# Optimization experiments

Measured on AMD Instinct MI355X. Metric: run time of the kernel, lower is better.

Reference implementation:

```python
import jax, jax.numpy as jnp
import numpy as np

B, T, V, E, H, O = 4096, 5, 8192, 32, 512, 1024
LN_EPS = 1e-5


def _ln(x, g, b):
    m = x.mean(-1, keepdims=True)
    v = x.var(-1, keepdims=True)
    return (x - m) / jnp.sqrt(v + LN_EPS) * g + b


def setup_inputs() -> dict:
    key = jax.random.key(0)
    ks = jax.random.split(key, 8)
    s_emb = 1.0 / np.sqrt(V)
    s_gru = 1.0 / np.sqrt(H)
    s_fc = 1.0 / np.sqrt(H)
    return {
        "message": jax.random.normal(ks[0], (B, T, V), jnp.float32),
        "emb_W": jax.random.normal(ks[1], (E, V), jnp.float32) * s_emb,
        "emb_b": jnp.zeros((E,), jnp.float32),
        "init_emb": jax.random.normal(ks[2], (1, E), jnp.float32),
        "eln_g": jnp.ones((E,), jnp.float32),
        "eln_b": jnp.zeros((E,), jnp.float32),
        "Wih": jax.random.normal(ks[3], (3 * H, E), jnp.float32) * s_gru,
        "Whh": jax.random.normal(ks[4], (3 * H, H), jnp.float32) * s_gru,
        "bih": jnp.zeros((3 * H,), jnp.float32),
        "bhh": jnp.zeros((3 * H,), jnp.float32),
        "gln_g": jnp.ones((H,), jnp.float32),
        "gln_b": jnp.zeros((H,), jnp.float32),
        "fc_W": jax.random.normal(ks[5], (O, H), jnp.float32) * s_fc,
        "fc_b": jnp.zeros((O,), jnp.float32),
    }


def reference(message, emb_W, emb_b, init_emb, eln_g, eln_b,
              Wih, Whh, bih, bhh, gln_g, gln_b, fc_W, fc_b):
    # embed all message steps at once: [B, T, E]
    emb = _ln(jnp.einsum('btv,ev->bte', message, emb_W) + emb_b, eln_g, eln_b)
    # GRU input sequence: LN(initial_embedding), then embeddings of steps 0..T-2
    x0 = jnp.broadcast_to(_ln(init_emb, eln_g, eln_b), (B, E))
    xs = jnp.concatenate([x0[None], jnp.swapaxes(emb[:, :T - 1], 0, 1)], axis=0)  # [T, B, E]

    def step(h, x):
        gi = x @ Wih.T + bih            # [B, 3H]
        gh = h @ Whh.T + bhh            # [B, 3H]
        ir, iz, inn = jnp.split(gi, 3, axis=-1)
        hr, hz, hn = jnp.split(gh, 3, axis=-1)
        r = jax.nn.sigmoid(ir + hr)
        z = jax.nn.sigmoid(iz + hz)
        n = jnp.tanh(inn + r * hn)
        h_new = (1.0 - z) * n + z * h
        return h_new, None

    h_last, _ = jax.lax.scan(step, jnp.zeros((B, H), message.dtype), xs)
    # eval mode: GaussianDropout is identity
    return jax.nn.sigmoid(_ln(h_last, gln_g, gln_b) @ fc_W.T + fc_b)
```

## Files before the change

kernel.cpp:

```cpp
#include <hip/hip_runtime.h>
#include <hip/hip_bf16.h>
#include <math.h>


#define LN_EPS 1e-5f

typedef __attribute__((ext_vector_type(8))) short bf8;
typedef __attribute__((ext_vector_type(4))) float fx4;

__device__ __forceinline__ float bf2f(short s) {
    union { unsigned u; float f; } v;
    v.u = ((unsigned)(unsigned short)s) << 16;
    return v.f;
}
__device__ __forceinline__ short f2bf(float f) {
    union { __hip_bfloat16 h; unsigned short u; } v;
    v.h = __float2bfloat16(f);
    return (short)v.u;
}
__device__ __forceinline__ float sigmoidf(float x) { return 1.0f / (1.0f + expf(-x)); }

__global__ __launch_bounds__(256) void k_prep(
    const float* __restrict__ Whh, const float* __restrict__ Wih,
    const float* __restrict__ fcW, const float* __restrict__ embW,
    const float* __restrict__ init_emb, const float* __restrict__ eln_g,
    const float* __restrict__ eln_b,
    short* __restrict__ Whh_bf, short* __restrict__ Wih_bf,
    short* __restrict__ fcW_bf, short* __restrict__ embW_bf,
    short* __restrict__ x0v, short* __restrict__ h0)
{
    int gid = blockIdx.x * blockDim.x + threadIdx.x;
    int stride = gridDim.x * blockDim.x;
    for (int i = gid; i < 1536 * 512; i += stride) Whh_bf[i] = f2bf(Whh[i]);
    for (int i = gid; i < 1536 * 32;  i += stride) Wih_bf[i] = f2bf(Wih[i]);
    for (int i = gid; i < 1024 * 512; i += stride) fcW_bf[i] = f2bf(fcW[i]);
    for (int i = gid; i < 32 * 8192;  i += stride) embW_bf[i] = f2bf(embW[i]);
    int* h0i = (int*)h0;
    for (int i = gid; i < 4096 * 512 / 2; i += stride) h0i[i] = 0;
    if (blockIdx.x == 0 && threadIdx.x < 32) {
        float v = init_emb[threadIdx.x];
        float s = v, q = v * v;
        #pragma unroll
        for (int m = 1; m < 32; m <<= 1) { s += __shfl_xor(s, m); q += __shfl_xor(q, m); }
        float mean = s * (1.0f / 32.0f);
        float var  = q * (1.0f / 32.0f) - mean * mean;
        float rstd = rsqrtf(var + LN_EPS);
        x0v[threadIdx.x] = f2bf((v - mean) * rstd * eln_g[threadIdx.x] + eln_b[threadIdx.x]);
    }
}

__global__ __launch_bounds__(256) void k_embed(
    const float* __restrict__ msg, const short* __restrict__ embW_bf,
    const float* __restrict__ emb_b, const float* __restrict__ eln_g,
    const float* __restrict__ eln_b, short* __restrict__ xs)
{
    __shared__ float part[4][16][33];

    const int tid  = threadIdx.x;
    const int w    = tid >> 6;
    const int lane = tid & 63;
    const int m    = lane & 15;
    const int quad = lane >> 4;

    const int rg = blockIdx.x * 16 + m;
    const int b  = rg >> 2, t = rg & 3;
    const float* __restrict__ row = msg + (size_t)(b * 5 + t) * 8192;

    const short* __restrict__ bw0 = embW_bf + (size_t)m * 8192;
    const short* __restrict__ bw1 = embW_bf + (size_t)(16 + m) * 8192;

    fx4 acc0, acc1;
    #pragma unroll
    for (int j = 0; j < 4; ++j) { acc0[j] = 0.0f; acc1[j] = 0.0f; }

    const int kbeg = w * 2048;
    const int kend = kbeg + 2048;
    #pragma unroll 4
    for (int k0 = kbeg; k0 < kend; k0 += 32) {
        const int kq = k0 + quad * 8;
        float4 a0 = *(const float4*)(row + kq);
        float4 a1 = *(const float4*)(row + kq + 4);
        bf8 a;
        a[0] = f2bf(a0.x); a[1] = f2bf(a0.y); a[2] = f2bf(a0.z); a[3] = f2bf(a0.w);
        a[4] = f2bf(a1.x); a[5] = f2bf(a1.y); a[6] = f2bf(a1.z); a[7] = f2bf(a1.w);
        bf8 b0 = *(const bf8*)(bw0 + kq);
        bf8 b1 = *(const bf8*)(bw1 + kq);
        acc0 = __builtin_amdgcn_mfma_f32_16x16x32_bf16(a, b0, acc0, 0, 0, 0);
        acc1 = __builtin_amdgcn_mfma_f32_16x16x32_bf16(a, b1, acc1, 0, 0, 0);
    }

    #pragma unroll
    for (int r = 0; r < 4; ++r) {
        part[w][quad * 4 + r][m]      = acc0[r];
        part[w][quad * 4 + r][16 + m] = acc1[r];
    }
    __syncthreads();

    {
        const int rr = tid >> 5;
        const int c  = tid & 31;
        #pragma unroll
        for (int half = 0; half < 2; ++half) {
            const int r = rr + half * 8;
            float v = part[0][r][c] + part[1][r][c] + part[2][r][c] + part[3][r][c]
                    + emb_b[c];
            float s = v, q = v * v;
            #pragma unroll
            for (int msk = 1; msk < 32; msk <<= 1) {
                s += __shfl_xor(s, msk); q += __shfl_xor(q, msk);
            }
            float mean = s * (1.0f / 32.0f);
            float var  = q * (1.0f / 32.0f) - mean * mean;
            float rstd = rsqrtf(var + LN_EPS);
            const int rg2 = blockIdx.x * 16 + r;
            const int b2 = rg2 >> 2, t2 = rg2 & 3;
            xs[(size_t)(t2 + 1) * 131072 + (size_t)b2 * 32 + c] =
                f2bf((v - mean) * rstd * eln_g[c] + eln_b[c]);
        }
    }
}

__global__ __launch_bounds__(256) void k_gru_step(
    const short* __restrict__ x, int x_stride,
    const short* __restrict__ h_in, short* __restrict__ h_out,
    const short* __restrict__ Whh_bf, const short* __restrict__ Wih_bf,
    const float* __restrict__ bih, const float* __restrict__ bhh)
{
    __shared__ short Hs[64][72];
    __shared__ short Ws[96][72];
    __shared__ short Xs[64][40];
    __shared__ short WIs[96][40];

    const int tid  = threadIdx.x;
    const int wid  = tid >> 6;
    const int lane = tid & 63;
    const int m    = lane & 15;
    const int quad = lane >> 4;
    const int row0 = blockIdx.x * 64;
    const int j0   = blockIdx.y * 32;

    fx4 acc_h[6], acc_i[6];
    #pragma unroll
    for (int i = 0; i < 6; ++i)
        #pragma unroll
        for (int j = 0; j < 4; ++j) { acc_h[i][j] = 0.0f; acc_i[i][j] = 0.0f; }

    {
        int c = tid;
        int r = c >> 2, kp = (c & 3) * 8;
        const short* src = x + (size_t)(row0 + r) * x_stride + kp;
        *(bf8*)&Xs[r][kp] = *(const bf8*)src;
    }
    #pragma unroll
    for (int i = 0; i < 2; ++i) {
        int c = tid + i * 256;
        if (c < 384) {
            int n = c >> 2, kp = (c & 3) * 8;
            int s = n >> 5, jj = n & 31;
            int g = s * 512 + j0 + jj;
            *(bf8*)&WIs[n][kp] = *(const bf8*)(Wih_bf + (size_t)g * 32 + kp);
        }
    }

    for (int k0 = 0; k0 < 512; k0 += 64) {
        #pragma unroll
        for (int i = 0; i < 2; ++i) {
            int c = tid + i * 256;
            int r = c >> 3, kp = (c & 7) * 8;
            *(bf8*)&Hs[r][kp] = *(const bf8*)(h_in + (size_t)(row0 + r) * 512 + k0 + kp);
        }
        #pragma unroll
        for (int i = 0; i < 3; ++i) {
            int c = tid + i * 256;
            int n = c >> 3, kp = (c & 7) * 8;
            int s = n >> 5, jj = n & 31;
            int g = s * 512 + j0 + jj;
            *(bf8*)&Ws[n][kp] = *(const bf8*)(Whh_bf + (size_t)g * 512 + k0 + kp);
        }
        __syncthreads();
        #pragma unroll
        for (int kk = 0; kk < 64; kk += 32) {
            bf8 a = *(const bf8*)&Hs[wid * 16 + m][kk + quad * 8];
            #pragma unroll
            for (int nt = 0; nt < 6; ++nt) {
                bf8 b = *(const bf8*)&Ws[(nt >> 1) * 32 + (nt & 1) * 16 + m][kk + quad * 8];
                acc_h[nt] = __builtin_amdgcn_mfma_f32_16x16x32_bf16(a, b, acc_h[nt], 0, 0, 0);
            }
        }
        __syncthreads();
    }
    {
        bf8 a = *(const bf8*)&Xs[wid * 16 + m][quad * 8];
        #pragma unroll
        for (int nt = 0; nt < 6; ++nt) {
            bf8 b = *(const bf8*)&WIs[(nt >> 1) * 32 + (nt & 1) * 16 + m][quad * 8];
            acc_i[nt] = __builtin_amdgcn_mfma_f32_16x16x32_bf16(a, b, acc_i[nt], 0, 0, 0);
        }
    }
    #pragma unroll
    for (int nt = 0; nt < 2; ++nt) {
        #pragma unroll
        for (int r = 0; r < 4; ++r) {
            int j  = j0 + nt * 16 + m;
            int rg = row0 + wid * 16 + quad * 4 + r;
            float rpre = acc_i[0 + nt][r] + bih[j]        + acc_h[0 + nt][r] + bhh[j];
            float zpre = acc_i[2 + nt][r] + bih[512 + j]  + acc_h[2 + nt][r] + bhh[512 + j];
            float inn  = acc_i[4 + nt][r] + bih[1024 + j];
            float hn   = acc_h[4 + nt][r] + bhh[1024 + j];
            float rr = sigmoidf(rpre);
            float zz = sigmoidf(zpre);
            float nn = tanhf(inn + rr * hn);
            float ho = bf2f(h_in[(size_t)rg * 512 + j]);
            h_out[(size_t)rg * 512 + j] = f2bf((1.0f - zz) * nn + zz * ho);
        }
    }
}

__global__ __launch_bounds__(256) void k_hln(
    const short* __restrict__ h, const float* __restrict__ g,
    const float* __restrict__ b, short* __restrict__ hln)
{
    int wid = threadIdx.x >> 6, lane = threadIdx.x & 63;
    int row = blockIdx.x * 4 + wid;
    bf8 v = *(const bf8*)(h + (size_t)row * 512 + lane * 8);
    float f[8];
    float sum = 0.f, sq = 0.f;
    #pragma unroll
    for (int i = 0; i < 8; ++i) { f[i] = bf2f(v[i]); sum += f[i]; sq += f[i] * f[i]; }
    #pragma unroll
    for (int msk = 1; msk < 64; msk <<= 1) { sum += __shfl_xor(sum, msk); sq += __shfl_xor(sq, msk); }
    float mean = sum * (1.0f / 512.0f);
    float var  = sq * (1.0f / 512.0f) - mean * mean;
    float rstd = rsqrtf(var + LN_EPS);
    short o[8];
    #pragma unroll
    for (int i = 0; i < 8; ++i) {
        int col = lane * 8 + i;
        o[i] = f2bf((f[i] - mean) * rstd * g[col] + b[col]);
    }
    *(bf8*)(hln + (size_t)row * 512 + lane * 8) = *(bf8*)o;
}

__global__ __launch_bounds__(256) void k_fc(
    const short* __restrict__ hln, const short* __restrict__ fcW_bf,
    const float* __restrict__ fc_b, float* __restrict__ out)
{
    __shared__ short As[64][72];
    __shared__ short Bs[64][72];

    const int tid  = threadIdx.x;
    const int wid  = tid >> 6;
    const int lane = tid & 63;
    const int m    = lane & 15;
    const int quad = lane >> 4;
    const int row0 = blockIdx.x * 64;
    const int col0 = blockIdx.y * 64;

    fx4 acc[4];
    #pragma unroll
    for (int i = 0; i < 4; ++i)
        #pragma unroll
        for (int j = 0; j < 4; ++j) acc[i][j] = 0.0f;

    for (int k0 = 0; k0 < 512; k0 += 64) {
        #pragma unroll
        for (int i = 0; i < 2; ++i) {
            int c = tid + i * 256;
            int r = c >> 3, kp = (c & 7) * 8;
            *(bf8*)&As[r][kp] = *(const bf8*)(hln + (size_t)(row0 + r) * 512 + k0 + kp);
        }
        #pragma unroll
        for (int i = 0; i < 2; ++i) {
            int c = tid + i * 256;
            int n = c >> 3, kp = (c & 7) * 8;
            *(bf8*)&Bs[n][kp] = *(const bf8*)(fcW_bf + (size_t)(col0 + n) * 512 + k0 + kp);
        }
        __syncthreads();
        #pragma unroll
        for (int kk = 0; kk < 64; kk += 32) {
            bf8 a = *(const bf8*)&As[wid * 16 + m][kk + quad * 8];
            #pragma unroll
            for (int nt = 0; nt < 4; ++nt) {
                bf8 b = *(const bf8*)&Bs[nt * 16 + m][kk + quad * 8];
                acc[nt] = __builtin_amdgcn_mfma_f32_16x16x32_bf16(a, b, acc[nt], 0, 0, 0);
            }
        }
        __syncthreads();
    }
    #pragma unroll
    for (int nt = 0; nt < 4; ++nt) {
        #pragma unroll
        for (int r = 0; r < 4; ++r) {
            int col = col0 + nt * 16 + m;
            int rg  = row0 + wid * 16 + quad * 4 + r;
            float v = acc[nt][r] + fc_b[col];
            out[(size_t)rg * 1024 + col] = sigmoidf(v);
        }
    }
}

extern "C" void kernel_launch(void* const* d_in, const int* in_sizes, int n_in,
                              void* d_out, int out_size, void* d_ws, size_t ws_size,
                              hipStream_t stream)
{
    const float* msg      = (const float*)d_in[0];
    const float* embW     = (const float*)d_in[1];
    const float* emb_b    = (const float*)d_in[2];
    const float* init_emb = (const float*)d_in[3];
    const float* eln_g    = (const float*)d_in[4];
    const float* eln_b    = (const float*)d_in[5];
    const float* Wih      = (const float*)d_in[6];
    const float* Whh      = (const float*)d_in[7];
    const float* bih      = (const float*)d_in[8];
    const float* bhh      = (const float*)d_in[9];
    const float* gln_g    = (const float*)d_in[10];
    const float* gln_b    = (const float*)d_in[11];
    const float* fcW      = (const float*)d_in[12];
    const float* fc_b     = (const float*)d_in[13];
    float* out = (float*)d_out;

    short* base    = (short*)d_ws;
    short* Whh_bf  = base;
    short* Wih_bf  = Whh_bf + 1536 * 512;
    short* fcW_bf  = Wih_bf + 1536 * 32;
    short* embW_bf = fcW_bf + 1024 * 512;
    short* xs      = embW_bf + 32 * 8192;
    short* h0      = xs + 5 * 4096 * 32;
    short* h1      = h0 + 4096 * 512;
    short* hln     = h1 + 4096 * 512;
    short* x0v     = hln + 4096 * 512;

    k_prep<<<512, 256, 0, stream>>>(Whh, Wih, fcW, embW, init_emb, eln_g, eln_b,
                                    Whh_bf, Wih_bf, fcW_bf, embW_bf, x0v, h0);
    k_embed<<<1024, 256, 0, stream>>>(msg, embW_bf, emb_b, eln_g, eln_b, xs);

    short* hi = h0;
    short* ho = h1;
    for (int t = 0; t < 5; ++t) {
        const short* xp = (t == 0) ? x0v : xs + (size_t)t * 4096 * 32;
        int xstride = (t == 0) ? 0 : 32;
        k_gru_step<<<dim3(64, 16), 256, 0, stream>>>(xp, xstride, hi, ho,
                                                     Whh_bf, Wih_bf, bih, bhh);
        short* tmp = hi; hi = ho; ho = tmp;
    }
    k_hln<<<1024, 256, 0, stream>>>(hi, gln_g, gln_b, hln);
    k_fc<<<dim3(64, 16), 256, 0, stream>>>(hln, fcW_bf, fc_b, out);
}
```

Baseline: 948.6 us.

## Drop LDS staging in GRU and FC GEMMs, load MFMA operands directly from global

```diff
diff --git a/kernel.cpp b/kernel.cpp
--- a/kernel.cpp
+++ b/kernel.cpp
@@ -126,11 +126,6 @@
     const short* __restrict__ Whh_bf, const short* __restrict__ Wih_bf,
     const float* __restrict__ bih, const float* __restrict__ bhh)
 {
-    __shared__ short Hs[64][72];
-    __shared__ short Ws[96][72];
-    __shared__ short Xs[64][40];
-    __shared__ short WIs[96][40];
-
     const int tid  = threadIdx.x;
     const int wid  = tid >> 6;
     const int lane = tid & 63;
@@ -139,64 +134,42 @@
     const int row0 = blockIdx.x * 64;
     const int j0   = blockIdx.y * 32;
 
+    const short* __restrict__ arow =
+        h_in + (size_t)(row0 + wid * 16 + m) * 512 + quad * 8;
+
+    const short* bw[6];
+    #pragma unroll
+    for (int nt = 0; nt < 6; ++nt) {
+        int g = (nt >> 1) * 512 + j0 + (nt & 1) * 16 + m;
+        bw[nt] = Whh_bf + (size_t)g * 512 + quad * 8;
+    }
+
     fx4 acc_h[6], acc_i[6];
     #pragma unroll
     for (int i = 0; i < 6; ++i)
         #pragma unroll
         for (int j = 0; j < 4; ++j) { acc_h[i][j] = 0.0f; acc_i[i][j] = 0.0f; }
 
+    #pragma unroll 2
+    for (int k = 0; k < 512; k += 32) {
+        bf8 a = *(const bf8*)(arow + k);
+        #pragma unroll
+        for (int nt = 0; nt < 6; ++nt) {
+            bf8 b = *(const bf8*)(bw[nt] + k);
+            acc_h[nt] = __builtin_amdgcn_mfma_f32_16x16x32_bf16(a, b, acc_h[nt], 0, 0, 0);
+        }
+    }
+
     {
-        int c = tid;
-        int r = c >> 2, kp = (c & 3) * 8;
-        const short* src = x + (size_t)(row0 + r) * x_stride + kp;
-        *(bf8*)&Xs[r][kp] = *(const bf8*)src;
-    }
-    #pragma unroll
-    for (int i = 0; i < 2; ++i) {
-        int c = tid + i * 256;
-        if (c < 384) {
-            int n = c >> 2, kp = (c & 3) * 8;
-            int s = n >> 5, jj = n & 31;
-            int g = s * 512 + j0 + jj;
-            *(bf8*)&WIs[n][kp] = *(const bf8*)(Wih_bf + (size_t)g * 32 + kp);
-        }
-    }
-
-    for (int k0 = 0; k0 < 512; k0 += 64) {
-        #pragma unroll
-        for (int i = 0; i < 2; ++i) {
-            int c = tid + i * 256;
-            int r = c >> 3, kp = (c & 7) * 8;
-            *(bf8*)&Hs[r][kp] = *(const bf8*)(h_in + (size_t)(row0 + r) * 512 + k0 + kp);
-        }
-        #pragma unroll
-        for (int i = 0; i < 3; ++i) {
-            int c = tid + i * 256;
-            int n = c >> 3, kp = (c & 7) * 8;
-            int s = n >> 5, jj = n & 31;
-            int g = s * 512 + j0 + jj;
-            *(bf8*)&Ws[n][kp] = *(const bf8*)(Whh_bf + (size_t)g * 512 + k0 + kp);
-        }
-        __syncthreads();
-        #pragma unroll
-        for (int kk = 0; kk < 64; kk += 32) {
-            bf8 a = *(const bf8*)&Hs[wid * 16 + m][kk + quad * 8];
-            #pragma unroll
-            for (int nt = 0; nt < 6; ++nt) {
-                bf8 b = *(const bf8*)&Ws[(nt >> 1) * 32 + (nt & 1) * 16 + m][kk + quad * 8];
-                acc_h[nt] = __builtin_amdgcn_mfma_f32_16x16x32_bf16(a, b, acc_h[nt], 0, 0, 0);
-            }
-        }
-        __syncthreads();
-    }
-    {
-        bf8 a = *(const bf8*)&Xs[wid * 16 + m][quad * 8];
+        bf8 a = *(const bf8*)(x + (size_t)(row0 + wid * 16 + m) * x_stride + quad * 8);
         #pragma unroll
         for (int nt = 0; nt < 6; ++nt) {
-            bf8 b = *(const bf8*)&WIs[(nt >> 1) * 32 + (nt & 1) * 16 + m][quad * 8];
+            int g = (nt >> 1) * 512 + j0 + (nt & 1) * 16 + m;
+            bf8 b = *(const bf8*)(Wih_bf + (size_t)g * 32 + quad * 8);
             acc_i[nt] = __builtin_amdgcn_mfma_f32_16x16x32_bf16(a, b, acc_i[nt], 0, 0, 0);
         }
     }
+
     #pragma unroll
     for (int nt = 0; nt < 2; ++nt) {
         #pragma unroll
@@ -245,9 +218,6 @@
     const short* __restrict__ hln, const short* __restrict__ fcW_bf,
     const float* __restrict__ fc_b, float* __restrict__ out)
 {
-    __shared__ short As[64][72];
-    __shared__ short Bs[64][72];
-
     const int tid  = threadIdx.x;
     const int wid  = tid >> 6;
     const int lane = tid & 63;
@@ -256,37 +226,29 @@
     const int row0 = blockIdx.x * 64;
     const int col0 = blockIdx.y * 64;
 
+    const short* __restrict__ arow =
+        hln + (size_t)(row0 + wid * 16 + m) * 512 + quad * 8;
+    const short* bw[4];
+    #pragma unroll
+    for (int nt = 0; nt < 4; ++nt)
+        bw[nt] = fcW_bf + (size_t)(col0 + nt * 16 + m) * 512 + quad * 8;
+
     fx4 acc[4];
     #pragma unroll
     for (int i = 0; i < 4; ++i)
         #pragma unroll
         for (int j = 0; j < 4; ++j) acc[i][j] = 0.0f;
 
-    for (int k0 = 0; k0 < 512; k0 += 64) {
-        #pragma unroll
-        for (int i = 0; i < 2; ++i) {
-            int c = tid + i * 256;
-            int r = c >> 3, kp = (c & 7) * 8;
-            *(bf8*)&As[r][kp] = *(const bf8*)(hln + (size_t)(row0 + r) * 512 + k0 + kp);
-        }
-        #pragma unroll
-        for (int i = 0; i < 2; ++i) {
-            int c = tid + i * 256;
-            int n = c >> 3, kp = (c & 7) * 8;
-            *(bf8*)&Bs[n][kp] = *(const bf8*)(fcW_bf + (size_t)(col0 + n) * 512 + k0 + kp);
-        }
-        __syncthreads();
-        #pragma unroll
-        for (int kk = 0; kk < 64; kk += 32) {
-            bf8 a = *(const bf8*)&As[wid * 16 + m][kk + quad * 8];
-            #pragma unroll
-            for (int nt = 0; nt < 4; ++nt) {
-                bf8 b = *(const bf8*)&Bs[nt * 16 + m][kk + quad * 8];
-                acc[nt] = __builtin_amdgcn_mfma_f32_16x16x32_bf16(a, b, acc[nt], 0, 0, 0);
-            }
-        }
-        __syncthreads();
-    }
+    #pragma unroll 2
+    for (int k = 0; k < 512; k += 32) {
+        bf8 a = *(const bf8*)(arow + k);
+        #pragma unroll
+        for (int nt = 0; nt < 4; ++nt) {
+            bf8 b = *(const bf8*)(bw[nt] + k);
+            acc[nt] = __builtin_amdgcn_mfma_f32_16x16x32_bf16(a, b, acc[nt], 0, 0, 0);
+        }
+    }
+
     #pragma unroll
     for (int nt = 0; nt < 4; ++nt) {
         #pragma unroll
```

New measurement: 1.196 ms. 26.1% more time.
